# Kernel tuning notes

Hardware: AMD Instinct MI355X
Metric: run time of the kernel (lower is better)

Reference implementation:

```python
import jax, jax.numpy as jnp
import numpy as np

DIM = 768
NUM_HEADS = 12
HEAD_DIM = DIM // NUM_HEADS
SCALE = HEAD_DIM ** -0.5


def setup_inputs() -> dict:
    key = jax.random.key(0)
    ks = jax.random.split(key, 7)
    B, N, C = 8, 1024, DIM
    x = jax.random.normal(ks[0], (B, N, C), dtype=jnp.float32)
    mask = jax.random.randint(ks[1], (B, N), 0, 2) > 0  # True = masked out
    qkv_w = jax.random.normal(ks[2], (3 * C, C), dtype=jnp.float32) * 0.02
    q_bias = jax.random.normal(ks[3], (C,), dtype=jnp.float32) * 0.02
    v_bias = jax.random.normal(ks[4], (C,), dtype=jnp.float32) * 0.02
    proj_w = jax.random.normal(ks[5], (C, C), dtype=jnp.float32) * 0.02
    proj_b = jax.random.normal(ks[6], (C,), dtype=jnp.float32) * 0.02
    return {"x": x, "mask": mask, "qkv_w": qkv_w, "q_bias": q_bias,
            "v_bias": v_bias, "proj_w": proj_w, "proj_b": proj_b}


def reference(x, mask, qkv_w, q_bias, v_bias, proj_w, proj_b):
    B, N, C = x.shape
    # CAE bias: concat(q_bias, zeros, v_bias) for the fused qkv projection
    qkv_bias = jnp.concatenate([q_bias, jnp.zeros_like(v_bias), v_bias])
    qkv = x @ qkv_w.T + qkv_bias  # [B, N, 3C]
    qkv = qkv.reshape(B, N, 3, NUM_HEADS, HEAD_DIM)
    q, k, v = (qkv[:, :, i].transpose(0, 2, 1, 3) for i in range(3))  # [B,H,N,hd]
    attn = jnp.einsum('bhqd,bhkd->bhqk', q * SCALE, k)  # [B,H,N,N]
    attn = jnp.where(mask[:, None, None, :], -jnp.inf, attn)
    attn = jax.nn.softmax(attn, axis=-1)
    out = jnp.einsum('bhqk,bhkd->bhqd', attn, v)  # [B,H,N,hd]
    out = out.transpose(0, 2, 1, 3).reshape(B, N, C)
    return out @ proj_w.T + proj_b
```

## Files before the change

kernel.cpp:

```cpp
#include <hip/hip_runtime.h>
#include <cstddef>
#include <cstdint>


typedef __attribute__((ext_vector_type(4))) float f32x4;
typedef __attribute__((ext_vector_type(8))) __bf16 bf16x8;
typedef __attribute__((ext_vector_type(4))) unsigned int uint4v;
typedef __attribute__((ext_vector_type(2))) unsigned int uint2v;

#define QK_PRESCALE 0.18033688011112042f

__device__ __forceinline__ unsigned short f2bf(float f) {
  return (unsigned short)((__float_as_uint(f) + 0x8000u) >> 16);
}
__device__ __forceinline__ unsigned int pack2bf(float flo, float fhi) {
  unsigned ulo = __float_as_uint(flo) + 0x8000u;
  unsigned uhi = __float_as_uint(fhi) + 0x8000u;
  return __builtin_amdgcn_perm(uhi, ulo, 0x07060302);
}

__device__ __forceinline__ void gl_lds16(const unsigned short* g, unsigned short* l) {
  __builtin_amdgcn_global_load_lds(
      (const __attribute__((address_space(1))) unsigned int*)g,
      (__attribute__((address_space(3))) unsigned int*)l, 16, 0, 0);
}

__global__ __launch_bounds__(256)
void cvt3_kernel(const float* __restrict__ s0, unsigned short* __restrict__ d0,
                 const float* __restrict__ s1, unsigned short* __restrict__ d1,
                 const float* __restrict__ s2, unsigned short* __restrict__ d2) {
  int bid = blockIdx.x;
  const float* s; unsigned short* d; int i; int n4;
  if (bid < 6144)      { s = s0; d = d0; i = bid * 256 + threadIdx.x;            n4 = 1572864; }
  else if (bid < 7872) { s = s1; d = d1; i = (bid - 6144) * 256 + threadIdx.x;   n4 = 442368; }
  else                 { s = s2; d = d2; i = (bid - 7872) * 256 + threadIdx.x;   n4 = 147456; }
  if (i < n4) {
    float4 v = ((const float4*)s)[i];
    uint2v o;
    o.x = pack2bf(v.x, v.y);
    o.y = pack2bf(v.z, v.w);
    ((uint2v*)d)[i] = o;
  }
}

__global__ __launch_bounds__(512, 2)
void qkv_gemm(const unsigned short* __restrict__ xb, const unsigned short* __restrict__ wb,
              const float* __restrict__ qb, const float* __restrict__ vb,
              unsigned short* __restrict__ qo, unsigned short* __restrict__ ko,
              unsigned short* __restrict__ vto) {
  __shared__ __align__(16) unsigned short lds[65536];
  const int tid = threadIdx.x;
  const int lane = tid & 63, wid = tid >> 6;
  const int lm = lane & 15, lq = lane >> 4;
  const int xsw = lm & 7;
  const int wr = wid >> 2, wc = wid & 3;
  const int L = blockIdx.x;
  const int xcd = L & 7, s = L >> 3;
  const int tt = xcd * 4 + s / 9;
  const int ft = s % 9;
  const int m0 = tt * 256;
  const int n0 = ft * 256;
  const int srow = lane >> 3;
  const int scolsw = ((lane & 7) ^ srow) * 8;
  const int laG = wr * 128 + wc * 16;
  const int lbG = (wid >> 1) * 64 + (wid & 1) * 16;
  const unsigned short* pa = wb + (size_t)(n0 + laG + srow) * 768 + scolsw;
  const unsigned short* pb = xb + (size_t)(m0 + lbG + srow) * 768 + scolsw;

  f32x4 acc[8][4] = {};

#define STAGE_A(g, tgt) { \
    const unsigned short* _s = pa + (size_t)(g) * 64 * 768 + (size_t)(tgt) * 64; \
    unsigned short* _d = &lds[(((tgt) & 1) * 256 + laG + (g) * 64) * 64]; \
    gl_lds16(_s, _d); \
    gl_lds16(_s + (size_t)8 * 768, _d + 8 * 64); }

#define STAGE_B(g, tgt) { \
    const unsigned short* _s = pb + (size_t)(g) * 32 * 768 + (size_t)(tgt) * 64; \
    unsigned short* _d = &lds[32768 + (((tgt) & 1) * 256 + lbG + (g) * 32) * 64]; \
    gl_lds16(_s, _d); \
    gl_lds16(_s + (size_t)8 * 768, _d + 8 * 64); }

#define PHASE_COMPUTE(qA, qB, bufb) { \
    const unsigned short* _Ab = &lds[(bufb) * 16384]; \
    const unsigned short* _Bb = &lds[32768 + (bufb) * 16384]; \
    bf16x8 af[4][2], bff[2][2]; \
    _Pragma("unroll") for (int m2 = 0; m2 < 4; ++m2) \
      _Pragma("unroll") for (int kx = 0; kx < 2; ++kx) \
        af[m2][kx] = *(const bf16x8*)&_Ab[(wr * 128 + ((qA) * 4 + m2) * 16 + lm) * 64 + (((kx * 4 + lq) ^ xsw) * 8)]; \
    _Pragma("unroll") for (int n2 = 0; n2 < 2; ++n2) \
      _Pragma("unroll") for (int kx = 0; kx < 2; ++kx) \
        bff[n2][kx] = *(const bf16x8*)&_Bb[(wc * 64 + ((qB) * 2 + n2) * 16 + lm) * 64 + (((kx * 4 + lq) ^ xsw) * 8)]; \
    __builtin_amdgcn_s_setprio(1); \
    _Pragma("unroll") for (int kx = 0; kx < 2; ++kx) \
      _Pragma("unroll") for (int m2 = 0; m2 < 4; ++m2) \
        _Pragma("unroll") for (int n2 = 0; n2 < 2; ++n2) \
          acc[(qA) * 4 + m2][(qB) * 2 + n2] = __builtin_amdgcn_mfma_f32_16x16x32_bf16( \
              af[m2][kx], bff[n2][kx], acc[(qA) * 4 + m2][(qB) * 2 + n2], 0, 0, 0); \
    __builtin_amdgcn_s_setprio(0); }

#define BAR_A_VM10() asm volatile("s_waitcnt vmcnt(10)\ns_barrier" ::: "memory")
#define BAR_A_VM8()  asm volatile("s_waitcnt vmcnt(8)\ns_barrier" ::: "memory")
#define BAR_A()      asm volatile("s_barrier" ::: "memory")
#define BAR_B()      asm volatile("s_waitcnt lgkmcnt(0)\ns_barrier" ::: "memory")

  STAGE_A(0, 0); STAGE_B(0, 0); STAGE_A(1, 0); STAGE_B(1, 0);
  STAGE_A(0, 1); STAGE_B(0, 1);

  for (int t = 0; t < 12; ++t) {
    const int b = t & 1;
    const int t1c = (t + 1 < 12) ? t + 1 : 11;
    const int t2c = (t + 2 < 12) ? t + 2 : 11;
    STAGE_A(1, t1c);
    BAR_A_VM10();
    PHASE_COMPUTE(0, 0, b);
    BAR_B();
    STAGE_B(1, t1c);
    BAR_A_VM8();
    PHASE_COMPUTE(0, 1, b);
    BAR_B();
    STAGE_A(0, t2c);
    BAR_A();
    PHASE_COMPUTE(1, 0, b);
    BAR_B();
    STAGE_B(0, t2c);
    BAR_A();
    PHASE_COMPUTE(1, 1, b);
    BAR_B();
  }
  asm volatile("s_waitcnt vmcnt(0)" ::: "memory");

#undef STAGE_A
#undef STAGE_B
#undef PHASE_COMPUTE

  const int bq = tt >> 2;
  const int tokb = (tt & 3) * 256;
  if (ft < 6) {
    const bool isq = ft < 3;
    unsigned short* dst0 = isq ? qo : ko;
    const int fbase = (isq ? ft : ft - 3) * 256 + wr * 128;
#pragma unroll
    for (int mi = 0; mi < 8; ++mi) {
      const int dg = fbase + mi * 16 + lq * 4;
      const int hh = dg >> 6;
      const int dih = dg & 63;
      f32x4 bias4 = {0.f, 0.f, 0.f, 0.f};
      if (isq) bias4 = *(const f32x4*)&qb[ft * 256 + wr * 128 + mi * 16 + lq * 4];
#pragma unroll
      for (int ni = 0; ni < 4; ++ni) {
        const int tok = tokb + wc * 64 + ni * 16 + lm;
        uint2v pk;
        if (isq) {
          pk.x = pack2bf((acc[mi][ni][0] + bias4[0]) * QK_PRESCALE,
                         (acc[mi][ni][1] + bias4[1]) * QK_PRESCALE);
          pk.y = pack2bf((acc[mi][ni][2] + bias4[2]) * QK_PRESCALE,
                         (acc[mi][ni][3] + bias4[3]) * QK_PRESCALE);
        } else {
          pk.x = pack2bf(acc[mi][ni][0], acc[mi][ni][1]);
          pk.y = pack2bf(acc[mi][ni][2], acc[mi][ni][3]);
        }
        *(uint2v*)&dst0[(((size_t)(bq * 12 + hh)) * 1024 + tok) * 64 + dih] = pk;
      }
    }
  } else {
    const int vb0 = (ft - 6) * 256;
    unsigned short* scr = lds;
#pragma unroll
    for (int p = 0; p < 2; ++p) {
      __syncthreads();
      if (wr == p) {
#pragma unroll
        for (int mi = 0; mi < 8; ++mi) {
          f32x4 bias4 = *(const f32x4*)&vb[vb0 + p * 128 + mi * 16 + lq * 4];
#pragma unroll
          for (int ni = 0; ni < 4; ++ni) {
            const int tok = wc * 64 + ni * 16 + lm;
#pragma unroll
            for (int r = 0; r < 4; ++r)
              scr[(mi * 16 + lq * 4 + r) * 264 + tok] = f2bf(acc[mi][ni][r] + bias4[r]);
          }
        }
      }
      __syncthreads();
      {
        const int row = tid >> 2, tq = tid & 3;
        const int dgv = vb0 + p * 128 + row;
        const int hh = dgv >> 6, d = dgv & 63;
        unsigned short* dstv = vto + (((size_t)(bq * 12 + hh)) * 64 + d) * 1024 + tokb + tq * 64;
        const unsigned short* srcr = &scr[row * 264 + tq * 64];
#pragma unroll
        for (int j = 0; j < 8; ++j)
          *(uint4v*)&dstv[j * 8] = *(const uint4v*)&srcr[j * 8];
      }
    }
  }
}

__global__ __launch_bounds__(256)
void attn_mfma(const unsigned short* __restrict__ q, const unsigned short* __restrict__ k,
               const unsigned short* __restrict__ vt, const int* __restrict__ mask,
               unsigned short* __restrict__ ao) {
  __shared__ unsigned short ks_s[64 * 64];
  __shared__ unsigned short vs_s[64 * 64];
  __shared__ unsigned short ps[4][32 * 72];
  __shared__ float mkl[64];
  const int tid = threadIdx.x;
  const int lane = tid & 63, wid = tid >> 6;
  const int lm = lane & 15, lq = lane >> 4;
  const int xsw = lm & 7;
  const int L = blockIdx.x;
  const int xcd = L & 7, s = L >> 3;
  const int bh = xcd * 12 + s / 8;
  const int qt = s % 8;
  const int bb = bh / 12, hh = bh % 12;
  const unsigned short* qp = q + (size_t)bh * 65536;
  const unsigned short* kp = k + (size_t)bh * 65536;
  const unsigned short* vp = vt + (size_t)bh * 65536;
  const int* mp = mask + bb * 1024;
  const int q0 = qt * 128 + wid * 32;
  const int srow = lane >> 3;
  const int scolsw = ((lane & 7) ^ srow) * 8;
  const unsigned short* gk = kp + (size_t)(wid * 16 + srow) * 64 + scolsw;
  const unsigned short* gv = vp + (size_t)(wid * 16 + srow) * 1024 + scolsw;

  bf16x8 qf[2][2];
#pragma unroll
  for (int mi = 0; mi < 2; ++mi)
#pragma unroll
    for (int ks2 = 0; ks2 < 2; ++ks2)
      qf[mi][ks2] = *(const bf16x8*)&qp[(size_t)(q0 + mi * 16 + lm) * 64 + ks2 * 32 + lq * 8];
  bf16x8 ones;
#pragma unroll
  for (int i = 0; i < 8; ++i) ones[i] = (__bf16)1.0f;

  f32x4 o_acc[2][4] = {};
  f32x4 l_acc[2] = {};

  for (int kt = 0; kt < 16; ++kt) {
    __syncthreads();
#pragma unroll
    for (int i = 0; i < 2; ++i) {
      gl_lds16(gk + (size_t)kt * 4096 + (size_t)i * 8 * 64, &ks_s[(wid * 16 + i * 8) * 64]);
      gl_lds16(gv + (size_t)kt * 64 + (size_t)i * 8 * 1024, &vs_s[(wid * 16 + i * 8) * 64]);
    }
    if (tid < 64) mkl[tid] = mp[kt * 64 + tid] ? -1e30f : 0.0f;
    __syncthreads();

    f32x4 st[4][2] = {};
#pragma unroll
    for (int ks2 = 0; ks2 < 2; ++ks2) {
      bf16x8 kf[4];
#pragma unroll
      for (int nt = 0; nt < 4; ++nt)
        kf[nt] = *(const bf16x8*)&ks_s[(nt * 16 + lm) * 64 + (((ks2 * 4 + lq) ^ xsw) * 8)];
#pragma unroll
      for (int nt = 0; nt < 4; ++nt)
#pragma unroll
        for (int mi = 0; mi < 2; ++mi)
          st[nt][mi] = __builtin_amdgcn_mfma_f32_16x16x32_bf16(kf[nt], qf[mi][ks2], st[nt][mi], 0, 0, 0);
    }

#pragma unroll
    for (int nt = 0; nt < 4; ++nt) {
      f32x4 mv4 = *(const f32x4*)&mkl[nt * 16 + lq * 4];
#pragma unroll
      for (int mi = 0; mi < 2; ++mi) {
        uint2v pk;
        pk.x = pack2bf(__builtin_amdgcn_exp2f(st[nt][mi][0] + mv4[0]),
                       __builtin_amdgcn_exp2f(st[nt][mi][1] + mv4[1]));
        pk.y = pack2bf(__builtin_amdgcn_exp2f(st[nt][mi][2] + mv4[2]),
                       __builtin_amdgcn_exp2f(st[nt][mi][3] + mv4[3]));
        *(uint2v*)&ps[wid][(mi * 16 + lm) * 72 + nt * 16 + lq * 4] = pk;
      }
    }

#pragma unroll
    for (int ks2 = 0; ks2 < 2; ++ks2) {
      bf16x8 pf[2], vf[4];
#pragma unroll
      for (int mi = 0; mi < 2; ++mi)
        pf[mi] = *(const bf16x8*)&ps[wid][(mi * 16 + lm) * 72 + ks2 * 32 + lq * 8];
#pragma unroll
      for (int nt = 0; nt < 4; ++nt)
        vf[nt] = *(const bf16x8*)&vs_s[(nt * 16 + lm) * 64 + (((ks2 * 4 + lq) ^ xsw) * 8)];
#pragma unroll
      for (int mi = 0; mi < 2; ++mi) {
#pragma unroll
        for (int nt = 0; nt < 4; ++nt)
          o_acc[mi][nt] = __builtin_amdgcn_mfma_f32_16x16x32_bf16(pf[mi], vf[nt], o_acc[mi][nt], 0, 0, 0);
        l_acc[mi] = __builtin_amdgcn_mfma_f32_16x16x32_bf16(pf[mi], ones, l_acc[mi], 0, 0, 0);
      }
    }
  }

#pragma unroll
  for (int mi = 0; mi < 2; ++mi) {
#pragma unroll
    for (int r = 0; r < 4; ++r) {
      float inv = 1.0f / l_acc[mi][r];
      int tok = q0 + mi * 16 + lq * 4 + r;
#pragma unroll
      for (int nt = 0; nt < 4; ++nt)
        ao[(size_t)(bb * 1024 + tok) * 768 + hh * 64 + nt * 16 + lm] = f2bf(o_acc[mi][nt][r] * inv);
    }
  }
}

__global__ __launch_bounds__(256)
void proj_gemm(const unsigned short* __restrict__ ab, const unsigned short* __restrict__ wb,
               const float* __restrict__ pb, float* __restrict__ out) {
  __shared__ unsigned short as[128 * 64];
  __shared__ unsigned short bs[128 * 64];
  const int tid = threadIdx.x;
  const int lane = tid & 63, wid = tid >> 6;
  const int lm = lane & 15, lq = lane >> 4;
  const int xsw = lm & 7;
  const int wm = (wid & 1) * 64, wn = (wid >> 1) * 64;
  const int L = blockIdx.x;
  const int xcd = L & 7, s = L >> 3;
  const int m0 = (xcd * 8 + s / 6) * 128;
  const int n0 = (s % 6) * 128;
  const int srow = lane >> 3;
  const int scolsw = ((lane & 7) ^ srow) * 8;
  const unsigned short* ga = wb + (size_t)(n0 + wid * 32 + srow) * 768 + scolsw;
  const unsigned short* gb = ab + (size_t)(m0 + wid * 32 + srow) * 768 + scolsw;
  f32x4 acc[4][4] = {};
  for (int kt = 0; kt < 768; kt += 64) {
#pragma unroll
    for (int i = 0; i < 4; ++i) {
      gl_lds16(ga + kt + (size_t)i * 8 * 768, &as[(wid * 32 + i * 8) * 64]);
      gl_lds16(gb + kt + (size_t)i * 8 * 768, &bs[(wid * 32 + i * 8) * 64]);
    }
    __syncthreads();
#pragma unroll
    for (int ks = 0; ks < 2; ++ks) {
      bf16x8 af[4], bf[4];
#pragma unroll
      for (int i = 0; i < 4; ++i)
        af[i] = *(const bf16x8*)&as[(wm + i * 16 + lm) * 64 + (((ks * 4 + lq) ^ xsw) * 8)];
#pragma unroll
      for (int i = 0; i < 4; ++i)
        bf[i] = *(const bf16x8*)&bs[(wn + i * 16 + lm) * 64 + (((ks * 4 + lq) ^ xsw) * 8)];
#pragma unroll
      for (int mi = 0; mi < 4; ++mi)
#pragma unroll
        for (int ni = 0; ni < 4; ++ni)
          acc[mi][ni] = __builtin_amdgcn_mfma_f32_16x16x32_bf16(af[mi], bf[ni], acc[mi][ni], 0, 0, 0);
    }
    __syncthreads();
  }
#pragma unroll
  for (int mi = 0; mi < 4; ++mi) {
    int gn0 = n0 + wm + mi * 16 + lq * 4;
    f32x4 bias4 = *(const f32x4*)&pb[gn0];
#pragma unroll
    for (int ni = 0; ni < 4; ++ni) {
      int gm = m0 + wn + ni * 16 + lm;
      f32x4 o;
      o[0] = acc[mi][ni][0] + bias4[0];
      o[1] = acc[mi][ni][1] + bias4[1];
      o[2] = acc[mi][ni][2] + bias4[2];
      o[3] = acc[mi][ni][3] + bias4[3];
      *(f32x4*)&out[(size_t)gm * 768 + gn0] = o;
    }
  }
}

extern "C" void kernel_launch(void* const* d_in, const int* in_sizes, int n_in,
                              void* d_out, int out_size, void* d_ws, size_t ws_size,
                              hipStream_t stream) {
  const float* x      = (const float*)d_in[0];
  const int*   mask   = (const int*)d_in[1];
  const float* qkv_w  = (const float*)d_in[2];
  const float* q_bias = (const float*)d_in[3];
  const float* v_bias = (const float*)d_in[4];
  const float* proj_w = (const float*)d_in[5];
  const float* proj_b = (const float*)d_in[6];
  float* out = (float*)d_out;
  unsigned short* p = (unsigned short*)d_ws;
  unsigned short* xb     = p;              p += 6291456;
  unsigned short* wqkvb  = p;              p += 1769472;
  unsigned short* wprojb = p;              p += 589824;
  unsigned short* qo     = p;              p += 6291456;
  unsigned short* ko     = p;              p += 6291456;
  unsigned short* vto    = p;              p += 6291456;
  unsigned short* ao     = p;

  cvt3_kernel<<<8448, 256, 0, stream>>>(x, xb, qkv_w, wqkvb, proj_w, wprojb);
  qkv_gemm<<<288, 512, 0, stream>>>(xb, wqkvb, q_bias, v_bias, qo, ko, vto);
  attn_mfma<<<768, 256, 0, stream>>>(qo, ko, vto, mask, ao);
  proj_gemm<<<384, 256, 0, stream>>>(ao, wprojb, proj_b, out);
}
```

Baseline: 205.1 us.

## Retile QKV GEMM to 288-wide feature tiles so grid matches 256 CUs

```diff
diff --git a/kernel.cpp b/kernel.cpp
--- a/kernel.cpp
+++ b/kernel.cpp
@@ -43,110 +43,131 @@
   }
 }
 
+__device__ __forceinline__ int a0row(int o) { return (o < 10) ? o * 8 : 144 + (o - 10) * 8; }
+__device__ __forceinline__ int a1row(int o) { return (o < 8) ? 80 + o * 8 : 224 + (o - 8) * 8; }
+
 __global__ __launch_bounds__(512, 2)
 void qkv_gemm(const unsigned short* __restrict__ xb, const unsigned short* __restrict__ wb,
               const float* __restrict__ qb, const float* __restrict__ vb,
               unsigned short* __restrict__ qo, unsigned short* __restrict__ ko,
               unsigned short* __restrict__ vto) {
-  __shared__ __align__(16) unsigned short lds[65536];
+  __shared__ __align__(16) unsigned short lds[69632];
   const int tid = threadIdx.x;
   const int lane = tid & 63, wid = tid >> 6;
+  const int widu = __builtin_amdgcn_readfirstlane(wid);
   const int lm = lane & 15, lq = lane >> 4;
   const int xsw = lm & 7;
-  const int wr = wid >> 2, wc = wid & 3;
+  const int wr = widu >> 2, wc = widu & 3;
   const int L = blockIdx.x;
   const int xcd = L & 7, s = L >> 3;
-  const int tt = xcd * 4 + s / 9;
-  const int ft = s % 9;
+  const int tt = xcd * 4 + (s >> 3);
+  const int ft = s & 7;
   const int m0 = tt * 256;
-  const int n0 = ft * 256;
+  const int n0 = ft * 288;
   const int srow = lane >> 3;
   const int scolsw = ((lane & 7) ^ srow) * 8;
-  const int laG = wr * 128 + wc * 16;
-  const int lbG = (wid >> 1) * 64 + (wid & 1) * 16;
-  const unsigned short* pa = wb + (size_t)(n0 + laG + srow) * 768 + scolsw;
-  const unsigned short* pb = xb + (size_t)(m0 + lbG + srow) * 768 + scolsw;
-
-  f32x4 acc[8][4] = {};
-
-#define STAGE_A(g, tgt) { \
-    const unsigned short* _s = pa + (size_t)(g) * 64 * 768 + (size_t)(tgt) * 64; \
-    unsigned short* _d = &lds[(((tgt) & 1) * 256 + laG + (g) * 64) * 64]; \
-    gl_lds16(_s, _d); \
-    gl_lds16(_s + (size_t)8 * 768, _d + 8 * 64); }
-
-#define STAGE_B(g, tgt) { \
-    const unsigned short* _s = pb + (size_t)(g) * 32 * 768 + (size_t)(tgt) * 64; \
-    unsigned short* _d = &lds[32768 + (((tgt) & 1) * 256 + lbG + (g) * 32) * 64]; \
-    gl_lds16(_s, _d); \
-    gl_lds16(_s + (size_t)8 * 768, _d + 8 * 64); }
-
-#define PHASE_COMPUTE(qA, qB, bufb) { \
-    const unsigned short* _Ab = &lds[(bufb) * 16384]; \
-    const unsigned short* _Bb = &lds[32768 + (bufb) * 16384]; \
-    bf16x8 af[4][2], bff[2][2]; \
-    _Pragma("unroll") for (int m2 = 0; m2 < 4; ++m2) \
+  const unsigned short* paS = wb + (size_t)(n0 + srow) * 768 + scolsw;
+  const unsigned short* pbS = xb + (size_t)(m0 + srow) * 768 + scolsw;
+
+  const int a0n3 = (widu < 4);
+  const int a0o = a0n3 ? widu * 3 : 12 + (widu - 4) * 2;
+  const int a0r0 = a0row(a0o), a0r1 = a0row(a0o + 1);
+  const int a0r2 = a0n3 ? a0row(a0o + 2) : 0;
+  const int a1r0 = a1row(2 * widu), a1r1 = a1row(2 * widu + 1);
+  const int b0q0 = (2 * widu) >> 2, b0q1 = (2 * widu + 1) >> 2;
+  const int b0r0 = b0q0 * 64 + ((2 * widu) & 3) * 8;
+  const int b0r1 = b0q1 * 64 + ((2 * widu + 1) & 3) * 8;
+  const int b1r0 = b0r0 + 32, b1r1 = b0r1 + 32;
+
+  f32x4 acc[9][4] = {};
+
+#define STAGE_A0(tgt) { const size_t _c = (size_t)(tgt) * 64; const int _b = ((tgt) & 1) * 18432; \
+    gl_lds16(paS + (size_t)a0r0 * 768 + _c, &lds[_b + a0r0 * 64]); \
+    gl_lds16(paS + (size_t)a0r1 * 768 + _c, &lds[_b + a0r1 * 64]); \
+    if (a0n3) gl_lds16(paS + (size_t)a0r2 * 768 + _c, &lds[_b + a0r2 * 64]); }
+
+#define STAGE_A1(tgt) { const size_t _c = (size_t)(tgt) * 64; const int _b = ((tgt) & 1) * 18432; \
+    gl_lds16(paS + (size_t)a1r0 * 768 + _c, &lds[_b + a1r0 * 64]); \
+    gl_lds16(paS + (size_t)a1r1 * 768 + _c, &lds[_b + a1r1 * 64]); }
+
+#define STAGE_B0(tgt) { const size_t _c = (size_t)(tgt) * 64; const int _b = 36864 + ((tgt) & 1) * 16384; \
+    gl_lds16(pbS + (size_t)b0r0 * 768 + _c, &lds[_b + b0r0 * 64]); \
+    gl_lds16(pbS + (size_t)b0r1 * 768 + _c, &lds[_b + b0r1 * 64]); }
+
+#define STAGE_B1(tgt) { const size_t _c = (size_t)(tgt) * 64; const int _b = 36864 + ((tgt) & 1) * 16384; \
+    gl_lds16(pbS + (size_t)b1r0 * 768 + _c, &lds[_b + b1r0 * 64]); \
+    gl_lds16(pbS + (size_t)b1r1 * 768 + _c, &lds[_b + b1r1 * 64]); }
+
+#define PHASE_COMPUTE(R0, NR, CB, bufb) { \
+    const unsigned short* _Ab = &lds[(bufb) * 18432]; \
+    const unsigned short* _Bb = &lds[36864 + (bufb) * 16384]; \
+    bf16x8 af[NR][2], bff[2][2]; \
+    _Pragma("unroll") for (int m2 = 0; m2 < (NR); ++m2) \
       _Pragma("unroll") for (int kx = 0; kx < 2; ++kx) \
-        af[m2][kx] = *(const bf16x8*)&_Ab[(wr * 128 + ((qA) * 4 + m2) * 16 + lm) * 64 + (((kx * 4 + lq) ^ xsw) * 8)]; \
+        af[m2][kx] = *(const bf16x8*)&_Ab[(wr * 144 + ((R0) + m2) * 16 + lm) * 64 + (((kx * 4 + lq) ^ xsw) * 8)]; \
     _Pragma("unroll") for (int n2 = 0; n2 < 2; ++n2) \
       _Pragma("unroll") for (int kx = 0; kx < 2; ++kx) \
-        bff[n2][kx] = *(const bf16x8*)&_Bb[(wc * 64 + ((qB) * 2 + n2) * 16 + lm) * 64 + (((kx * 4 + lq) ^ xsw) * 8)]; \
+        bff[n2][kx] = *(const bf16x8*)&_Bb[(wc * 64 + ((CB) * 2 + n2) * 16 + lm) * 64 + (((kx * 4 + lq) ^ xsw) * 8)]; \
     __builtin_amdgcn_s_setprio(1); \
     _Pragma("unroll") for (int kx = 0; kx < 2; ++kx) \
-      _Pragma("unroll") for (int m2 = 0; m2 < 4; ++m2) \
+      _Pragma("unroll") for (int m2 = 0; m2 < (NR); ++m2) \
         _Pragma("unroll") for (int n2 = 0; n2 < 2; ++n2) \
-          acc[(qA) * 4 + m2][(qB) * 2 + n2] = __builtin_amdgcn_mfma_f32_16x16x32_bf16( \
-              af[m2][kx], bff[n2][kx], acc[(qA) * 4 + m2][(qB) * 2 + n2], 0, 0, 0); \
+          acc[(R0) + m2][(CB) * 2 + n2] = __builtin_amdgcn_mfma_f32_16x16x32_bf16( \
+              af[m2][kx], bff[n2][kx], acc[(R0) + m2][(CB) * 2 + n2], 0, 0, 0); \
     __builtin_amdgcn_s_setprio(0); }
 
-#define BAR_A_VM10() asm volatile("s_waitcnt vmcnt(10)\ns_barrier" ::: "memory")
-#define BAR_A_VM8()  asm volatile("s_waitcnt vmcnt(8)\ns_barrier" ::: "memory")
-#define BAR_A()      asm volatile("s_barrier" ::: "memory")
-#define BAR_B()      asm volatile("s_waitcnt lgkmcnt(0)\ns_barrier" ::: "memory")
-
-  STAGE_A(0, 0); STAGE_B(0, 0); STAGE_A(1, 0); STAGE_B(1, 0);
-  STAGE_A(0, 1); STAGE_B(0, 1);
+#define WAIT_Q0() { if (a0n3) asm volatile("s_waitcnt vmcnt(7)" ::: "memory"); \
+                    else      asm volatile("s_waitcnt vmcnt(6)" ::: "memory"); \
+                    asm volatile("s_barrier" ::: "memory"); }
+#define WAIT_Q1() { if (a0n3) asm volatile("s_waitcnt vmcnt(5)" ::: "memory"); \
+                    else      asm volatile("s_waitcnt vmcnt(4)" ::: "memory"); \
+                    asm volatile("s_barrier" ::: "memory"); }
+#define BAR_A()   asm volatile("s_barrier" ::: "memory")
+#define BAR_B()   asm volatile("s_waitcnt lgkmcnt(0)\ns_barrier" ::: "memory")
+
+  STAGE_A0(0); STAGE_B0(0); STAGE_A1(0); STAGE_B1(0);
 
   for (int t = 0; t < 12; ++t) {
     const int b = t & 1;
-    const int t1c = (t + 1 < 12) ? t + 1 : 11;
-    const int t2c = (t + 2 < 12) ? t + 2 : 11;
-    STAGE_A(1, t1c);
-    BAR_A_VM10();
-    PHASE_COMPUTE(0, 0, b);
+    const int tn = (t < 11) ? t + 1 : 11;
+    STAGE_A0(tn);
+    WAIT_Q0();
+    PHASE_COMPUTE(0, 5, 0, b);
     BAR_B();
-    STAGE_B(1, t1c);
-    BAR_A_VM8();
-    PHASE_COMPUTE(0, 1, b);
+    STAGE_B0(tn);
+    WAIT_Q1();
+    PHASE_COMPUTE(0, 5, 1, b);
     BAR_B();
-    STAGE_A(0, t2c);
+    STAGE_A1(tn);
     BAR_A();
-    PHASE_COMPUTE(1, 0, b);
+    PHASE_COMPUTE(5, 4, 0, b);
     BAR_B();
-    STAGE_B(0, t2c);
+    STAGE_B1(tn);
     BAR_A();
-    PHASE_COMPUTE(1, 1, b);
+    PHASE_COMPUTE(5, 4, 1, b);
     BAR_B();
   }
   asm volatile("s_waitcnt vmcnt(0)" ::: "memory");
 
-#undef STAGE_A
-#undef STAGE_B
+#undef STAGE_A0
+#undef STAGE_A1
+#undef STAGE_B0
+#undef STAGE_B1
 #undef PHASE_COMPUTE
 
   const int bq = tt >> 2;
   const int tokb = (tt & 3) * 256;
-  if (ft < 6) {
-    const bool isq = ft < 3;
-    unsigned short* dst0 = isq ? qo : ko;
-    const int fbase = (isq ? ft : ft - 3) * 256 + wr * 128;
-#pragma unroll
-    for (int mi = 0; mi < 8; ++mi) {
-      const int dg = fbase + mi * 16 + lq * 4;
-      const int hh = dg >> 6;
-      const int dih = dg & 63;
+#pragma unroll
+  for (int mi = 0; mi < 9; ++mi) {
+    const int fblk = n0 + wr * 144 + mi * 16;
+    if (fblk < 1536) {
+      const bool isq = fblk < 768;
+      unsigned short* dst0 = isq ? qo : ko;
+      const int fd = fblk - (isq ? 0 : 768);
+      const int hh = fd >> 6;
+      const int dih = (fd & 63) + lq * 4;
       f32x4 bias4 = {0.f, 0.f, 0.f, 0.f};
-      if (isq) bias4 = *(const f32x4*)&qb[ft * 256 + wr * 128 + mi * 16 + lq * 4];
+      if (isq) bias4 = *(const f32x4*)&qb[fblk + lq * 4];
 #pragma unroll
       for (int ni = 0; ni < 4; ++ni) {
         const int tok = tokb + wc * 64 + ni * 16 + lm;
@@ -163,32 +184,36 @@
         *(uint2v*)&dst0[(((size_t)(bq * 12 + hh)) * 1024 + tok) * 64 + dih] = pk;
       }
     }
-  } else {
-    const int vb0 = (ft - 6) * 256;
-    unsigned short* scr = lds;
+  }
+  if (n0 + 288 > 1536) {
 #pragma unroll
     for (int p = 0; p < 2; ++p) {
       __syncthreads();
       if (wr == p) {
 #pragma unroll
-        for (int mi = 0; mi < 8; ++mi) {
-          f32x4 bias4 = *(const f32x4*)&vb[vb0 + p * 128 + mi * 16 + lq * 4];
-#pragma unroll
-          for (int ni = 0; ni < 4; ++ni) {
-            const int tok = wc * 64 + ni * 16 + lm;
-#pragma unroll
-            for (int r = 0; r < 4; ++r)
-              scr[(mi * 16 + lq * 4 + r) * 264 + tok] = f2bf(acc[mi][ni][r] + bias4[r]);
+        for (int mi = 0; mi < 9; ++mi) {
+          const int fblk = n0 + p * 144 + mi * 16;
+          if (fblk >= 1536) {
+            f32x4 bias4 = *(const f32x4*)&vb[fblk - 1536 + lq * 4];
+#pragma unroll
+            for (int ni = 0; ni < 4; ++ni) {
+              const int tokl = wc * 64 + ni * 16 + lm;
+#pragma unroll
+              for (int r = 0; r < 4; ++r)
+                lds[(mi * 16 + lq * 4 + r) * 264 + tokl] = f2bf(acc[mi][ni][r] + bias4[r]);
+            }
           }
         }
       }
       __syncthreads();
-      {
-        const int row = tid >> 2, tq = tid & 3;
-        const int dgv = vb0 + p * 128 + row;
+      const int fv = 1536 - (n0 + p * 144);
+      const int rv0 = fv > 0 ? fv : 0;
+      for (int r = rv0 + (tid >> 2); r < 144; r += 128) {
+        const int tq = tid & 3;
+        const int dgv = n0 + p * 144 + r - 1536;
         const int hh = dgv >> 6, d = dgv & 63;
         unsigned short* dstv = vto + (((size_t)(bq * 12 + hh)) * 64 + d) * 1024 + tokb + tq * 64;
-        const unsigned short* srcr = &scr[row * 264 + tq * 64];
+        const unsigned short* srcr = &lds[r * 264 + tq * 64];
 #pragma unroll
         for (int j = 0; j < 8; ++j)
           *(uint4v*)&dstv[j * 8] = *(const uint4v*)&srcr[j * 8];
@@ -388,7 +413,7 @@
   unsigned short* ao     = p;
 
   cvt3_kernel<<<8448, 256, 0, stream>>>(x, xb, qkv_w, wqkvb, proj_w, wprojb);
-  qkv_gemm<<<288, 512, 0, stream>>>(xb, wqkvb, q_bias, v_bias, qo, ko, vto);
+  qkv_gemm<<<256, 512, 0, stream>>>(xb, wqkvb, q_bias, v_bias, qo, ko, vto);
   attn_mfma<<<768, 256, 0, stream>>>(qo, ko, vto, mask, ao);
   proj_gemm<<<384, 256, 0, stream>>>(ao, wprojb, proj_b, out);
 }
```

Result: faster. 184.3 us (-10.1%).
